# Optimization experiments

Measured on AMD Instinct MI355X. Metric: run time of the kernel, lower is better.

Reference implementation:

```python
import jax, jax.numpy as jnp
import numpy as np


def setup_inputs() -> dict:
    key = jax.random.key(0)
    kx, ky, kz = jax.random.split(key, 3)
    x = jax.random.normal(kx, (32, 2048, 1024), dtype=jnp.float32)
    y = jax.random.normal(ky, (8, 32, 2048, 64), dtype=jnp.float32)
    z = jax.random.normal(kz, (32, 4096, 512), dtype=jnp.float32)
    return {"x": x, "y": y, "z": z}


def reference(x, y, z):
    # torch.topk(x, 4): top-4 largest along last dim, sorted descending
    x_top, _ = jax.lax.top_k(x, 4)  # [32, 2048, 4]

    # torch.topk(y, k=1, dim=2, largest=False): single smallest along dim 2.
    # Move dim 2 to last, take top-1 of the negation, negate back.
    y_m = jnp.moveaxis(y, 2, -1)              # [8, 32, 64, 2048]
    y_min = -jax.lax.top_k(-y_m, 1)[0]        # [8, 32, 64, 1]
    y_min = jnp.moveaxis(y_min, -1, 2)        # [8, 32, 1, 64]

    # torch.topk(z, k=3, dim=-1, sorted=False): top-3 values + indices.
    # (sorted=False allows any order; we return them sorted descending,
    # which is a valid ordering of the same selected set.)
    z_top, z_idx = jax.lax.top_k(z, 3)        # [32, 4096, 3] each

    return (x_top, y_min, z_top, z_idx)
```

## Files before the change

### kernel.cpp

```cpp
#include <hip/hip_runtime.h>

#define OUT_X  0
#define OUT_Y  262144
#define OUT_ZV 278528
#define OUT_ZI 671744


__device__ __forceinline__ void bub4(float &a0, float &a1, float &a2, float &a3, float v) {
    float r;
    r = fminf(a0, v); a0 = fmaxf(a0, v); v = r;
    r = fminf(a1, v); a1 = fmaxf(a1, v); v = r;
    r = fminf(a2, v); a2 = fmaxf(a2, v); v = r;
    a3 = fmaxf(a3, v);
}

__global__ __launch_bounds__(256) void topk_x_kernel(const float* __restrict__ x,
                                                     float* __restrict__ out) {
    const int lane = threadIdx.x & 63;
    const int row  = blockIdx.x * 4 + (threadIdx.x >> 6);
    const float4* r4 = (const float4*)(x + (size_t)row * 1024);

    float a0 = -3.402823466e38f, a1 = a0, a2 = a0, a3 = a0;
    #pragma unroll
    for (int c = 0; c < 4; ++c) {
        float4 v = r4[lane + 64 * c];
        bub4(a0, a1, a2, a3, v.x);
        bub4(a0, a1, a2, a3, v.y);
        bub4(a0, a1, a2, a3, v.z);
        bub4(a0, a1, a2, a3, v.w);
    }

    #pragma unroll
    for (int m = 1; m < 64; m <<= 1) {
        float b0 = __shfl_xor(a0, m, 64);
        float b1 = __shfl_xor(a1, m, 64);
        float b2 = __shfl_xor(a2, m, 64);
        float b3 = __shfl_xor(a3, m, 64);
        float m0 = fmaxf(a0, b3), m1 = fmaxf(a1, b2), m2 = fmaxf(a2, b1), m3 = fmaxf(a3, b0);
        float e0 = fmaxf(m0, m2), e2 = fminf(m0, m2);
        float e1 = fmaxf(m1, m3), e3 = fminf(m1, m3);
        a0 = fmaxf(e0, e1); a1 = fminf(e0, e1);
        a2 = fmaxf(e2, e3); a3 = fminf(e2, e3);
    }

    if (lane == 0) {
        ((float4*)(out + OUT_X))[row] = make_float4(a0, a1, a2, a3);
    }
}


__device__ __forceinline__ float4 min4(float4 a, float4 b) {
    return make_float4(fminf(a.x, b.x), fminf(a.y, b.y), fminf(a.z, b.z), fminf(a.w, b.w));
}

__global__ __launch_bounds__(1024) void ymin_kernel(const float* __restrict__ y,
                                                    float* __restrict__ out) {
    const int pair = blockIdx.x;
    const int c4 = threadIdx.x & 15;
    const int rg = threadIdx.x >> 4;
    const float4* base = (const float4*)(y + (size_t)pair * 2048 * 64);

    float4 m = make_float4(3.402823466e38f, 3.402823466e38f, 3.402823466e38f, 3.402823466e38f);
    #pragma unroll 4
    for (int r = rg; r < 2048; r += 64) {
        m = min4(m, base[r * 16 + c4]);
    }

    __shared__ float4 red[1024];
    red[threadIdx.x] = m;
    __syncthreads();
    #pragma unroll
    for (int s = 512; s >= 16; s >>= 1) {
        if (threadIdx.x < s) red[threadIdx.x] = min4(red[threadIdx.x], red[threadIdx.x + s]);
        __syncthreads();
    }
    if (threadIdx.x < 16) {
        ((float4*)(out + OUT_Y + pair * 64))[threadIdx.x] = red[threadIdx.x];
    }
}


__device__ __forceinline__ unsigned long long mkkey(float v, int idx) {
    unsigned int b = __float_as_uint(v);
    unsigned int u = b ^ ((unsigned int)((int)b >> 31) | 0x80000000u);
    return ((unsigned long long)u << 32) | (unsigned int)(511 - idx);
}

__device__ __forceinline__ void ins3(unsigned long long &k0, unsigned long long &k1,
                                     unsigned long long &k2, unsigned long long k) {
    unsigned long long t;
    t = (k0 > k) ? k : k0; k0 = (k0 > k) ? k0 : k; k = t;
    t = (k1 > k) ? k : k1; k1 = (k1 > k) ? k1 : k; k = t;
    k2 = (k2 > k) ? k2 : k;
}

__device__ __forceinline__ void ce64(unsigned long long &a, unsigned long long &b) {
    unsigned long long hi = (a > b) ? a : b;
    unsigned long long lo = (a > b) ? b : a;
    a = hi; b = lo;
}

__device__ __forceinline__ unsigned long long shfl_xor_u64(unsigned long long v, int mask) {
    unsigned int lo = (unsigned int)v;
    unsigned int hi = (unsigned int)(v >> 32);
    lo = __shfl_xor(lo, mask, 64);
    hi = __shfl_xor(hi, mask, 64);
    return ((unsigned long long)hi << 32) | lo;
}

__global__ __launch_bounds__(256) void topk_z_kernel(const float* __restrict__ z,
                                                     float* __restrict__ outv,
                                                     float* __restrict__ outi) {
    const int lane = threadIdx.x & 63;
    const int row  = blockIdx.x * 4 + (threadIdx.x >> 6);
    const float4* r4 = (const float4*)(z + (size_t)row * 512);

    unsigned long long k0 = 0ull, k1 = 0ull, k2 = 0ull;
    #pragma unroll
    for (int c = 0; c < 2; ++c) {
        int i = lane + 64 * c;
        float4 v = r4[i];
        int base = 4 * i;
        ins3(k0, k1, k2, mkkey(v.x, base));
        ins3(k0, k1, k2, mkkey(v.y, base + 1));
        ins3(k0, k1, k2, mkkey(v.z, base + 2));
        ins3(k0, k1, k2, mkkey(v.w, base + 3));
    }

    #pragma unroll
    for (int m = 1; m < 64; m <<= 1) {
        unsigned long long b0 = shfl_xor_u64(k0, m);
        unsigned long long b1 = shfl_xor_u64(k1, m);
        unsigned long long b2 = shfl_xor_u64(k2, m);
        unsigned long long m0 = (k0 > b2) ? k0 : b2;
        unsigned long long m1 = (k1 > b1) ? k1 : b1;
        unsigned long long m2 = (k2 > b0) ? k2 : b0;
        ce64(m0, m1); ce64(m1, m2); ce64(m0, m1);
        k0 = m0; k1 = m1; k2 = m2;
    }

    if (lane == 0) {
        unsigned long long ks[3] = {k0, k1, k2};
        #pragma unroll
        for (int j = 0; j < 3; ++j) {
            unsigned int u = (unsigned int)(ks[j] >> 32);
            unsigned int b = (u & 0x80000000u) ? (u ^ 0x80000000u) : ~u;
            outv[(size_t)row * 3 + j] = __uint_as_float(b);
            outi[(size_t)row * 3 + j] = (float)(511 - (int)(ks[j] & 0xFFFFFFFFu));
        }
    }
}

extern "C" void kernel_launch(void* const* d_in, const int* in_sizes, int n_in,
                              void* d_out, int out_size, void* d_ws, size_t ws_size,
                              hipStream_t stream) {
    const float* x = (const float*)d_in[0];
    const float* y = (const float*)d_in[1];
    const float* z = (const float*)d_in[2];
    float* out = (float*)d_out;

    topk_x_kernel<<<65536 / 4, 256, 0, stream>>>(x, out);
    ymin_kernel<<<256, 1024, 0, stream>>>(y, out);
    topk_z_kernel<<<131072 / 4, 256, 0, stream>>>(z, out + OUT_ZV, out + OUT_ZI);
}
```

Before: 601.6 us.

## Fuse three top-k kernels into one launch with nontemporal loads and split accumulators

Merges the x top-4, y column-min and z top-3 kernels into a single grid that picks its branch from the block index, with the small y reduction placed first so it overlaps the larger streams. All input reads become nontemporal loads, since each value is read only once. The per-thread insertion chains are split into two independent accumulators that are merged at the end, giving more instruction-level parallelism. The y path now uses 256-thread blocks, so each of its only 256 blocks does a longer loop per thread, which could leave it as a tail at the end of the grid.

```diff
diff --git a/kernel.cpp b/kernel.cpp
--- a/kernel.cpp
+++ b/kernel.cpp
@@ -4,6 +4,17 @@
 #define OUT_Y  262144
 #define OUT_ZV 278528
 #define OUT_ZI 671744
+
+#define YB 256
+#define ZB 32768
+#define XB 16384
+
+typedef float vf4 __attribute__((ext_vector_type(4)));
+
+__device__ __forceinline__ float4 ldnt4(const float4* p) {
+    vf4 v = __builtin_nontemporal_load((const vf4*)p);
+    return make_float4(v.x, v.y, v.z, v.w);
+}
 
 
 __device__ __forceinline__ void bub4(float &a0, float &a1, float &a2, float &a3, float v) {
@@ -14,69 +25,18 @@
     a3 = fmaxf(a3, v);
 }
 
-__global__ __launch_bounds__(256) void topk_x_kernel(const float* __restrict__ x,
-                                                     float* __restrict__ out) {
-    const int lane = threadIdx.x & 63;
-    const int row  = blockIdx.x * 4 + (threadIdx.x >> 6);
-    const float4* r4 = (const float4*)(x + (size_t)row * 1024);
-
-    float a0 = -3.402823466e38f, a1 = a0, a2 = a0, a3 = a0;
-    #pragma unroll
-    for (int c = 0; c < 4; ++c) {
-        float4 v = r4[lane + 64 * c];
-        bub4(a0, a1, a2, a3, v.x);
-        bub4(a0, a1, a2, a3, v.y);
-        bub4(a0, a1, a2, a3, v.z);
-        bub4(a0, a1, a2, a3, v.w);
-    }
-
-    #pragma unroll
-    for (int m = 1; m < 64; m <<= 1) {
-        float b0 = __shfl_xor(a0, m, 64);
-        float b1 = __shfl_xor(a1, m, 64);
-        float b2 = __shfl_xor(a2, m, 64);
-        float b3 = __shfl_xor(a3, m, 64);
-        float m0 = fmaxf(a0, b3), m1 = fmaxf(a1, b2), m2 = fmaxf(a2, b1), m3 = fmaxf(a3, b0);
-        float e0 = fmaxf(m0, m2), e2 = fminf(m0, m2);
-        float e1 = fmaxf(m1, m3), e3 = fminf(m1, m3);
-        a0 = fmaxf(e0, e1); a1 = fminf(e0, e1);
-        a2 = fmaxf(e2, e3); a3 = fminf(e2, e3);
-    }
-
-    if (lane == 0) {
-        ((float4*)(out + OUT_X))[row] = make_float4(a0, a1, a2, a3);
-    }
+__device__ __forceinline__ void merge4(float &a0, float &a1, float &a2, float &a3,
+                                       float b0, float b1, float b2, float b3) {
+    float m0 = fmaxf(a0, b3), m1 = fmaxf(a1, b2), m2 = fmaxf(a2, b1), m3 = fmaxf(a3, b0);
+    float e0 = fmaxf(m0, m2), e2 = fminf(m0, m2);
+    float e1 = fmaxf(m1, m3), e3 = fminf(m1, m3);
+    a0 = fmaxf(e0, e1); a1 = fminf(e0, e1);
+    a2 = fmaxf(e2, e3); a3 = fminf(e2, e3);
 }
 
 
 __device__ __forceinline__ float4 min4(float4 a, float4 b) {
     return make_float4(fminf(a.x, b.x), fminf(a.y, b.y), fminf(a.z, b.z), fminf(a.w, b.w));
-}
-
-__global__ __launch_bounds__(1024) void ymin_kernel(const float* __restrict__ y,
-                                                    float* __restrict__ out) {
-    const int pair = blockIdx.x;
-    const int c4 = threadIdx.x & 15;
-    const int rg = threadIdx.x >> 4;
-    const float4* base = (const float4*)(y + (size_t)pair * 2048 * 64);
-
-    float4 m = make_float4(3.402823466e38f, 3.402823466e38f, 3.402823466e38f, 3.402823466e38f);
-    #pragma unroll 4
-    for (int r = rg; r < 2048; r += 64) {
-        m = min4(m, base[r * 16 + c4]);
-    }
-
-    __shared__ float4 red[1024];
-    red[threadIdx.x] = m;
-    __syncthreads();
-    #pragma unroll
-    for (int s = 512; s >= 16; s >>= 1) {
-        if (threadIdx.x < s) red[threadIdx.x] = min4(red[threadIdx.x], red[threadIdx.x + s]);
-        __syncthreads();
-    }
-    if (threadIdx.x < 16) {
-        ((float4*)(out + OUT_Y + pair * 64))[threadIdx.x] = red[threadIdx.x];
-    }
 }
 
 
@@ -100,6 +60,17 @@
     a = hi; b = lo;
 }
 
+__device__ __forceinline__ void merge3(unsigned long long &a0, unsigned long long &a1,
+                                       unsigned long long &a2,
+                                       unsigned long long b0, unsigned long long b1,
+                                       unsigned long long b2) {
+    unsigned long long m0 = (a0 > b2) ? a0 : b2;
+    unsigned long long m1 = (a1 > b1) ? a1 : b1;
+    unsigned long long m2 = (a2 > b0) ? a2 : b0;
+    ce64(m0, m1); ce64(m1, m2); ce64(m0, m1);
+    a0 = m0; a1 = m1; a2 = m2;
+}
+
 __device__ __forceinline__ unsigned long long shfl_xor_u64(unsigned long long v, int mask) {
     unsigned int lo = (unsigned int)v;
     unsigned int hi = (unsigned int)(v >> 32);
@@ -108,45 +79,113 @@
     return ((unsigned long long)hi << 32) | lo;
 }
 
-__global__ __launch_bounds__(256) void topk_z_kernel(const float* __restrict__ z,
-                                                     float* __restrict__ outv,
-                                                     float* __restrict__ outi) {
-    const int lane = threadIdx.x & 63;
-    const int row  = blockIdx.x * 4 + (threadIdx.x >> 6);
-    const float4* r4 = (const float4*)(z + (size_t)row * 512);
-
-    unsigned long long k0 = 0ull, k1 = 0ull, k2 = 0ull;
-    #pragma unroll
-    for (int c = 0; c < 2; ++c) {
-        int i = lane + 64 * c;
-        float4 v = r4[i];
-        int base = 4 * i;
-        ins3(k0, k1, k2, mkkey(v.x, base));
-        ins3(k0, k1, k2, mkkey(v.y, base + 1));
-        ins3(k0, k1, k2, mkkey(v.z, base + 2));
-        ins3(k0, k1, k2, mkkey(v.w, base + 3));
-    }
-
-    #pragma unroll
-    for (int m = 1; m < 64; m <<= 1) {
-        unsigned long long b0 = shfl_xor_u64(k0, m);
-        unsigned long long b1 = shfl_xor_u64(k1, m);
-        unsigned long long b2 = shfl_xor_u64(k2, m);
-        unsigned long long m0 = (k0 > b2) ? k0 : b2;
-        unsigned long long m1 = (k1 > b1) ? k1 : b1;
-        unsigned long long m2 = (k2 > b0) ? k2 : b0;
-        ce64(m0, m1); ce64(m1, m2); ce64(m0, m1);
-        k0 = m0; k1 = m1; k2 = m2;
-    }
-
-    if (lane == 0) {
-        unsigned long long ks[3] = {k0, k1, k2};
+
+__global__ __launch_bounds__(256) void fused_topk_kernel(const float* __restrict__ x,
+                                                         const float* __restrict__ y,
+                                                         const float* __restrict__ z,
+                                                         float* __restrict__ out) {
+    const int bid = blockIdx.x;
+    const int tid = threadIdx.x;
+
+    if (bid < YB) {
+        const int pair = bid;
+        const int c4 = tid & 15;
+        const int rg = tid >> 4;
+        const float4* base = (const float4*)(y + (size_t)pair * 2048 * 64);
+
+        const float INF = 3.402823466e38f;
+        float4 m = make_float4(INF, INF, INF, INF);
+        #pragma unroll 8
+        for (int r = rg; r < 2048; r += 16) {
+            m = min4(m, ldnt4(base + r * 16 + c4));
+        }
+
+        __shared__ float4 red[256];
+        red[tid] = m;
+        __syncthreads();
         #pragma unroll
-        for (int j = 0; j < 3; ++j) {
-            unsigned int u = (unsigned int)(ks[j] >> 32);
-            unsigned int b = (u & 0x80000000u) ? (u ^ 0x80000000u) : ~u;
-            outv[(size_t)row * 3 + j] = __uint_as_float(b);
-            outi[(size_t)row * 3 + j] = (float)(511 - (int)(ks[j] & 0xFFFFFFFFu));
+        for (int s = 128; s >= 16; s >>= 1) {
+            if (tid < s) red[tid] = min4(red[tid], red[tid + s]);
+            __syncthreads();
+        }
+        if (tid < 16) {
+            ((float4*)(out + OUT_Y + pair * 64))[tid] = red[tid];
+        }
+    } else if (bid < YB + ZB) {
+        const int lane = tid & 63;
+        const int row  = (bid - YB) * 4 + (tid >> 6);
+        const float4* r4 = (const float4*)(z + (size_t)row * 512);
+
+        float4 v0 = ldnt4(r4 + lane);
+        float4 v1 = ldnt4(r4 + lane + 64);
+
+        unsigned long long a0 = 0ull, a1 = 0ull, a2 = 0ull;
+        unsigned long long b0 = 0ull, b1 = 0ull, b2 = 0ull;
+        int i0 = 4 * lane, i1 = 4 * (lane + 64);
+        ins3(a0, a1, a2, mkkey(v0.x, i0));
+        ins3(b0, b1, b2, mkkey(v1.x, i1));
+        ins3(a0, a1, a2, mkkey(v0.y, i0 + 1));
+        ins3(b0, b1, b2, mkkey(v1.y, i1 + 1));
+        ins3(a0, a1, a2, mkkey(v0.z, i0 + 2));
+        ins3(b0, b1, b2, mkkey(v1.z, i1 + 2));
+        ins3(a0, a1, a2, mkkey(v0.w, i0 + 3));
+        ins3(b0, b1, b2, mkkey(v1.w, i1 + 3));
+        merge3(a0, a1, a2, b0, b1, b2);
+
+        #pragma unroll
+        for (int m = 1; m < 64; m <<= 1) {
+            unsigned long long s0 = shfl_xor_u64(a0, m);
+            unsigned long long s1 = shfl_xor_u64(a1, m);
+            unsigned long long s2 = shfl_xor_u64(a2, m);
+            merge3(a0, a1, a2, s0, s1, s2);
+        }
+
+        if (lane == 0) {
+            unsigned long long ks[3] = {a0, a1, a2};
+            float* outv = out + OUT_ZV;
+            float* outi = out + OUT_ZI;
+            #pragma unroll
+            for (int j = 0; j < 3; ++j) {
+                unsigned int u = (unsigned int)(ks[j] >> 32);
+                unsigned int bb = (u & 0x80000000u) ? (u ^ 0x80000000u) : ~u;
+                outv[(size_t)row * 3 + j] = __uint_as_float(bb);
+                outi[(size_t)row * 3 + j] = (float)(511 - (int)(ks[j] & 0xFFFFFFFFu));
+            }
+        }
+    } else {
+        const int lane = tid & 63;
+        const int row  = (bid - YB - ZB) * 4 + (tid >> 6);
+        const float4* r4 = (const float4*)(x + (size_t)row * 1024);
+
+        float4 v0 = ldnt4(r4 + lane);
+        float4 v1 = ldnt4(r4 + lane + 64);
+        float4 v2 = ldnt4(r4 + lane + 128);
+        float4 v3 = ldnt4(r4 + lane + 192);
+
+        const float NINF = -3.402823466e38f;
+        float a0 = NINF, a1 = NINF, a2 = NINF, a3 = NINF;
+        float c0 = NINF, c1 = NINF, c2 = NINF, c3 = NINF;
+        bub4(a0, a1, a2, a3, v0.x); bub4(c0, c1, c2, c3, v2.x);
+        bub4(a0, a1, a2, a3, v0.y); bub4(c0, c1, c2, c3, v2.y);
+        bub4(a0, a1, a2, a3, v0.z); bub4(c0, c1, c2, c3, v2.z);
+        bub4(a0, a1, a2, a3, v0.w); bub4(c0, c1, c2, c3, v2.w);
+        bub4(a0, a1, a2, a3, v1.x); bub4(c0, c1, c2, c3, v3.x);
+        bub4(a0, a1, a2, a3, v1.y); bub4(c0, c1, c2, c3, v3.y);
+        bub4(a0, a1, a2, a3, v1.z); bub4(c0, c1, c2, c3, v3.z);
+        bub4(a0, a1, a2, a3, v1.w); bub4(c0, c1, c2, c3, v3.w);
+        merge4(a0, a1, a2, a3, c0, c1, c2, c3);
+
+        #pragma unroll
+        for (int m = 1; m < 64; m <<= 1) {
+            float s0 = __shfl_xor(a0, m, 64);
+            float s1 = __shfl_xor(a1, m, 64);
+            float s2 = __shfl_xor(a2, m, 64);
+            float s3 = __shfl_xor(a3, m, 64);
+            merge4(a0, a1, a2, a3, s0, s1, s2, s3);
+        }
+
+        if (lane == 0) {
+            ((float4*)(out + OUT_X))[row] = make_float4(a0, a1, a2, a3);
         }
     }
 }
@@ -159,7 +198,5 @@
     const float* z = (const float*)d_in[2];
     float* out = (float*)d_out;
 
-    topk_x_kernel<<<65536 / 4, 256, 0, stream>>>(x, out);
-    ymin_kernel<<<256, 1024, 0, stream>>>(y, out);
-    topk_z_kernel<<<131072 / 4, 256, 0, stream>>>(z, out + OUT_ZV, out + OUT_ZI);
-}
+    fused_topk_kernel<<<YB + ZB + XB, 256, 0, stream>>>(x, y, z, out);
+}
```

After: 564.7 us. -6.1%, faster.
